# Performance work log

Measured on AMD Instinct MI355X. Metric: run time of the kernel, lower is better.

## Reference

```python
import jax, jax.numpy as jnp
import numpy as np
from jax.scipy.linalg import expm

LATENT, HIDDEN, N_PARTS, K = 128, 2048, 128, 2048
OMEGA_DIM, TRANZ_DIM = 9 * N_PARTS, 3 * N_PARTS


def setup_inputs() -> dict:
    key = jax.random.key(0)
    ks = jax.random.split(key, 10)

    def w(k, out_d, in_d):
        # eqx.nn.Linear-style scale ~ 1/sqrt(fan_in)
        return jax.random.normal(k, (out_d, in_d), dtype=jnp.float32) / np.sqrt(in_d)

    return {
        "x_init": jax.random.normal(ks[0], (LATENT, K), dtype=jnp.float32),
        "Wo0": w(ks[1], HIDDEN, LATENT),
        "Wo1": w(ks[2], HIDDEN, HIDDEN),
        "Wo2": w(ks[3], HIDDEN, HIDDEN),
        "Wo3": w(ks[4], OMEGA_DIM, HIDDEN),
        "Wt0": w(ks[5], HIDDEN, LATENT),
        "Wt1": w(ks[6], HIDDEN, HIDDEN),
        "Wt2": w(ks[7], HIDDEN, HIDDEN),
        "Wt3": w(ks[8], TRANZ_DIM, HIDDEN),
    }


def _mlp(weights, x):
    # bias-free MLP, relu on all but last layer; x is (d_in, K)
    for i, W in enumerate(weights):
        x = W @ x
        if i + 1 < len(weights):
            x = jax.nn.relu(x)
    return x


def reference(x_init, Wo0, Wo1, Wo2, Wo3, Wt0, Wt1, Wt2, Wt3):
    omega = _mlp([Wo0, Wo1, Wo2, Wo3], x_init)            # (9n, K)
    n = omega.shape[0] // 9
    k = omega.shape[1]
    # exp_omega 2D branch: vmap over columns, each column -> (n,3,3) expm batch
    mats = omega.T.reshape(k * n, 3, 3)
    R = jax.vmap(expm)(mats).reshape(k, 9 * n)            # (K, 9n)
    rotations = R.T                                        # (9n, K)
    translations = _mlp([Wt0, Wt1, Wt2, Wt3], x_init)     # (3n, K)
    # form_transformations (2D branch): stack translation as a 4th row -> (12n, K)
    rot_r = rotations.reshape(n, 3, 3, k)
    tr_r = translations.reshape(n, 1, 3, k)
    transf = jnp.concatenate([rot_r, tr_r], axis=1).reshape(-1, k)  # (12n, K)
    return (omega, transf, rotations, translations)
```

## Files before the change

kernel.cpp:

```cpp
#include <hip/hip_runtime.h>
#include <stdint.h>


typedef short bf16x8 __attribute__((ext_vector_type(8)));
typedef float f32x4 __attribute__((ext_vector_type(4)));

__device__ __forceinline__ unsigned short f2bf(float f) {
  unsigned int x = __float_as_uint(f);
  unsigned int r = (x + 0x7fffu + ((x >> 16) & 1u)) >> 16;
  return (unsigned short)r;
}

__device__ __forceinline__ void gld_lds16(const void* g, void* l) {
  __builtin_amdgcn_global_load_lds(
      (__attribute__((address_space(1))) void*)(g),
      (__attribute__((address_space(3))) void*)(l),
      16, 0, 0);
}

__global__ void prep_k(const float* __restrict__ x,
                       const float* __restrict__ wo0, const float* __restrict__ wo1,
                       const float* __restrict__ wo2, const float* __restrict__ wo3,
                       const float* __restrict__ wt0, const float* __restrict__ wt1,
                       const float* __restrict__ wt2, const float* __restrict__ wt3,
                       unsigned short* __restrict__ dst, unsigned short* __restrict__ xt) {
  __shared__ float tile[32][33];
  const int b = blockIdx.x;
  const int tid = threadIdx.x;
  if (b >= 9984) {
    const int r = b - 9984;
    const int bx = r & 63, by = r >> 6;
    const int tx = tid & 31, ty = tid >> 5;
#pragma unroll
    for (int i = 0; i < 32; i += 8)
      tile[ty + i][tx] = x[(size_t)(by * 32 + ty + i) * 2048 + bx * 32 + tx];
    __syncthreads();
#pragma unroll
    for (int i = 0; i < 32; i += 8)
      xt[(size_t)(bx * 32 + ty + i) * 128 + by * 32 + tx] = f2bf(tile[tx][ty + i]);
    return;
  }
  int idx = (b * 256 + tid) * 8;
  if (idx >= 20447232) return;
  const float* src;
  int off;
  if (idx < 8650752) {
    if (idx < 262144)       { src = wo0; off = idx; }
    else if (idx < 4456448) { src = wo1; off = idx - 262144; }
    else                    { src = wo2; off = idx - 4456448; }
  } else {
    if (idx < 11010048)      { src = wo3; off = idx - 8650752; }
    else if (idx < 11272192) { src = wt0; off = idx - 11010048; }
    else if (idx < 15466496) { src = wt1; off = idx - 11272192; }
    else if (idx < 19660800) { src = wt2; off = idx - 15466496; }
    else                     { src = wt3; off = idx - 19660800; }
  }
  float4 a = *(const float4*)(src + off);
  float4 c = *(const float4*)(src + off + 4);
  uint4 o;
  o.x = (unsigned)f2bf(a.x) | ((unsigned)f2bf(a.y) << 16);
  o.y = (unsigned)f2bf(a.z) | ((unsigned)f2bf(a.w) << 16);
  o.z = (unsigned)f2bf(c.x) | ((unsigned)f2bf(c.y) << 16);
  o.w = (unsigned)f2bf(c.z) | ((unsigned)f2bf(c.w) << 16);
  *(uint4*)(dst + idx) = o;
}

template <int SWZ>
__global__ __launch_bounds__(256, 2) void gemm_tn(
    const unsigned short* __restrict__ A0, const unsigned short* __restrict__ B0,
    unsigned short* __restrict__ C0, int n0tiles, int ldc0,
    const unsigned short* __restrict__ A1, const unsigned short* __restrict__ B1,
    unsigned short* __restrict__ C1, int ldc1, int K) {
  __shared__ alignas(16) unsigned short Asl[128 * 128];
  __shared__ alignas(16) unsigned short Bsl[128 * 128];

  int mt, yt;
  if (SWZ) {
    int id = blockIdx.x;
    int xcd = id & 7, s = id >> 3;
    mt = ((xcd & 1) << 3) + (s & 7);
    yt = ((xcd >> 1) << 3) + (s >> 3);
  } else {
    mt = blockIdx.x;
    yt = blockIdx.y;
  }

  const unsigned short* A;
  const unsigned short* B;
  unsigned short* C;
  int ldc;
  if (yt < n0tiles) { A = A0; B = B0; C = C0; ldc = ldc0; }
  else { A = A1; B = B1; C = C1; ldc = ldc1; yt -= n0tiles; }

  const unsigned short* Ab = A + (size_t)mt * 128 * K;
  const unsigned short* Bb = B + (size_t)yt * 128 * K;

  const int tid = threadIdx.x;
  const int wave = tid >> 6, lane = tid & 63;
  const int mw = (wave >> 1) * 64, nw = (wave & 1) * 64;
  const int l16 = lane & 15, quad = lane >> 4;

  f32x4 acc[4][4] = {};

  for (int k0 = 0; k0 < K; k0 += 128) {
#pragma unroll
    for (int i = 0; i < 8; ++i) {
      int c = i * 256 + tid;
      int row = c >> 4;
      int l = (c & 15) ^ (row & 15);
      gld_lds16(Ab + (size_t)row * K + k0 + l * 8, &Asl[c * 8]);
      gld_lds16(Bb + (size_t)row * K + k0 + l * 8, &Bsl[c * 8]);
    }
    __syncthreads();

#pragma unroll
    for (int h = 0; h < 4; ++h) {
      bf16x8 af[4], bfr[4];
#pragma unroll
      for (int t = 0; t < 4; ++t) {
        int row = mw + t * 16 + l16;
        int p = (h * 4 + quad) ^ (row & 15);
        af[t] = *(const bf16x8*)&Asl[row * 128 + p * 8];
      }
#pragma unroll
      for (int t = 0; t < 4; ++t) {
        int row = nw + t * 16 + l16;
        int p = (h * 4 + quad) ^ (row & 15);
        bfr[t] = *(const bf16x8*)&Bsl[row * 128 + p * 8];
      }
#pragma unroll
      for (int tm = 0; tm < 4; ++tm)
#pragma unroll
        for (int tn = 0; tn < 4; ++tn)
          acc[tm][tn] = __builtin_amdgcn_mfma_f32_16x16x32_bf16(af[tm], bfr[tn], acc[tm][tn], 0, 0, 0);
    }
    __syncthreads();
  }

  const int mbase = mt * 128 + mw;
  const int nbase = yt * 128 + nw;
#pragma unroll
  for (int tm = 0; tm < 4; ++tm) {
#pragma unroll
    for (int tn = 0; tn < 4; ++tn) {
      int col = nbase + tn * 16 + l16;
      int row0 = mbase + tm * 16 + quad * 4;
#pragma unroll
      for (int r = 0; r < 4; ++r) {
        float v = fmaxf(acc[tm][tn][r], 0.0f);
        C[(size_t)(row0 + r) * ldc + col] = f2bf(v);
      }
    }
  }
}

__device__ __forceinline__ void mm3(const float* a, const float* b, float* c) {
#pragma unroll
  for (int r = 0; r < 3; ++r)
#pragma unroll
    for (int cc = 0; cc < 3; ++cc)
      c[r * 3 + cc] = a[r * 3 + 0] * b[0 + cc] + a[r * 3 + 1] * b[3 + cc] + a[r * 3 + 2] * b[6 + cc];
}

__device__ __forceinline__ void expm3(const float* a, float* E) {
  float n1 = 0.f;
#pragma unroll
  for (int c = 0; c < 3; ++c) {
    float s = fabsf(a[c]) + fabsf(a[3 + c]) + fabsf(a[6 + c]);
    n1 = fmaxf(n1, s);
  }
  int s = 0;
  if (n1 > 0.25f) {
    s = (int)ceilf(log2f(n1 * 4.0f));
    if (s < 0) s = 0;
  }
  const float scl = exp2f((float)(-s));
  float As[9];
#pragma unroll
  for (int i = 0; i < 9; ++i) As[i] = a[i] * scl;
  float T[9] = {1, 0, 0, 0, 1, 0, 0, 0, 1};
#pragma unroll
  for (int i = 0; i < 9; ++i) E[i] = T[i];
#pragma unroll
  for (int t = 1; t <= 12; ++t) {
    float Tn[9];
    mm3(T, As, Tn);
    const float inv = 1.0f / (float)t;
#pragma unroll
    for (int i = 0; i < 9; ++i) { T[i] = Tn[i] * inv; E[i] += T[i]; }
  }
  for (int q = 0; q < s; ++q) {
    float Tn[9];
    mm3(E, E, Tn);
#pragma unroll
    for (int i = 0; i < 9; ++i) E[i] = Tn[i];
  }
}

__global__ __launch_bounds__(256, 2) void gemm_l3(
    const unsigned short* __restrict__ Ho, const unsigned short* __restrict__ W9,
    const unsigned short* __restrict__ Ht, const unsigned short* __restrict__ W3,
    float* __restrict__ out) {
  __shared__ alignas(16) char smem[16384 + 39168];
  unsigned short* Asl = (unsigned short*)smem;
  unsigned short* Bsl = (unsigned short*)(smem + 16384);
  float* Cl = (float*)(smem + 16384);

  const int mt = blockIdx.x;
  const int yt = blockIdx.y;
  const int tid = threadIdx.x;
  const int wave = tid >> 6, lane = tid & 63;
  const int l16 = lane & 15, quad = lane >> 4;
  const int mbase = mt * 64;

  float* omega  = out;
  float* transf = out + (size_t)1152 * 2048;
  float* rot    = out + (size_t)(1152 + 1536) * 2048;
  float* transl = out + (size_t)(1152 + 1536 + 1152) * 2048;

  if (yt < 8) {
    const unsigned short* Ab = Ho + (size_t)mbase * 2048;
    const unsigned short* Bb = W9 + (size_t)yt * 144 * 2048;
    const int mw = wave * 16;
    f32x4 acc[9] = {};

    for (int k0 = 0; k0 < 2048; k0 += 128) {
#pragma unroll
      for (int i = 0; i < 4; ++i) {
        int c = i * 256 + tid;
        int row = c >> 4;
        int l = (c & 15) ^ (row & 15);
        gld_lds16(Ab + (size_t)row * 2048 + k0 + l * 8, &Asl[c * 8]);
      }
#pragma unroll
      for (int i = 0; i < 9; ++i) {
        int c = i * 256 + tid;
        int row = c >> 4;
        int l = (c & 15) ^ (row & 15);
        gld_lds16(Bb + (size_t)row * 2048 + k0 + l * 8, &Bsl[c * 8]);
      }
      __syncthreads();
#pragma unroll
      for (int h = 0; h < 4; ++h) {
        bf16x8 af;
        {
          int row = mw + l16;
          int p = (h * 4 + quad) ^ (row & 15);
          af = *(const bf16x8*)&Asl[row * 128 + p * 8];
        }
#pragma unroll
        for (int t = 0; t < 9; ++t) {
          int row = t * 16 + l16;
          int p = (h * 4 + quad) ^ (row & 15);
          bf16x8 bf = *(const bf16x8*)&Bsl[row * 128 + p * 8];
          acc[t] = __builtin_amdgcn_mfma_f32_16x16x32_bf16(af, bf, acc[t], 0, 0, 0);
        }
      }
      __syncthreads();
    }

#pragma unroll
    for (int t = 0; t < 9; ++t) {
      int d = t * 16 + l16;
      int s0 = mw + quad * 4;
      *(f32x4*)&Cl[d * 68 + s0] = acc[t];
    }
    __syncthreads();

    const int jbase = yt * 16;
    const int k = mbase + lane;
#pragma unroll 1
    for (int pp = 0; pp < 4; ++pp) {
      int pl = wave * 4 + pp;
      int j = jbase + pl;
      float a[9];
#pragma unroll
      for (int i = 0; i < 9; ++i) a[i] = Cl[(pl * 9 + i) * 68 + lane];
#pragma unroll
      for (int i = 0; i < 9; ++i) omega[(size_t)(9 * j + i) * 2048 + k] = a[i];
      float E[9];
      expm3(a, E);
#pragma unroll
      for (int i = 0; i < 9; ++i) {
        rot[(size_t)(9 * j + i) * 2048 + k] = E[i];
        transf[(size_t)(12 * j + i) * 2048 + k] = E[i];
      }
    }
  } else {
    const int nt = yt - 8;
    const unsigned short* Ab = Ht + (size_t)mbase * 2048;
    const unsigned short* Bb = W3 + (size_t)nt * 128 * 2048;
    const int mw = (wave >> 1) * 32, nw = (wave & 1) * 64;
    f32x4 acc[2][4] = {};

    for (int k0 = 0; k0 < 2048; k0 += 128) {
#pragma unroll
      for (int i = 0; i < 4; ++i) {
        int c = i * 256 + tid;
        int row = c >> 4;
        int l = (c & 15) ^ (row & 15);
        gld_lds16(Ab + (size_t)row * 2048 + k0 + l * 8, &Asl[c * 8]);
      }
#pragma unroll
      for (int i = 0; i < 8; ++i) {
        int c = i * 256 + tid;
        int row = c >> 4;
        int l = (c & 15) ^ (row & 15);
        gld_lds16(Bb + (size_t)row * 2048 + k0 + l * 8, &Bsl[c * 8]);
      }
      __syncthreads();
#pragma unroll
      for (int h = 0; h < 4; ++h) {
        bf16x8 af[2], bfr[4];
#pragma unroll
        for (int t = 0; t < 2; ++t) {
          int row = mw + t * 16 + l16;
          int p = (h * 4 + quad) ^ (row & 15);
          af[t] = *(const bf16x8*)&Asl[row * 128 + p * 8];
        }
#pragma unroll
        for (int t = 0; t < 4; ++t) {
          int row = nw + t * 16 + l16;
          int p = (h * 4 + quad) ^ (row & 15);
          bfr[t] = *(const bf16x8*)&Bsl[row * 128 + p * 8];
        }
#pragma unroll
        for (int tm = 0; tm < 2; ++tm)
#pragma unroll
          for (int tn = 0; tn < 4; ++tn)
            acc[tm][tn] = __builtin_amdgcn_mfma_f32_16x16x32_bf16(af[tm], bfr[tn], acc[tm][tn], 0, 0, 0);
      }
      __syncthreads();
    }

    const int nbase = nt * 128 + nw;
#pragma unroll
    for (int tm = 0; tm < 2; ++tm) {
#pragma unroll
      for (int tn = 0; tn < 4; ++tn) {
        int n = nbase + tn * 16 + l16;
        int row0 = mbase + mw + tm * 16 + quad * 4;
        int j = n / 3, c = n % 3;
        *(f32x4*)&transl[(size_t)n * 2048 + row0] = acc[tm][tn];
        *(f32x4*)&transf[(size_t)(12 * j + 9 + c) * 2048 + row0] = acc[tm][tn];
      }
    }
  }
}

extern "C" void kernel_launch(void* const* d_in, const int* in_sizes, int n_in,
                              void* d_out, int out_size, void* d_ws, size_t ws_size,
                              hipStream_t stream) {
  const float* x   = (const float*)d_in[0];
  const float* Wo0 = (const float*)d_in[1];
  const float* Wo1 = (const float*)d_in[2];
  const float* Wo2 = (const float*)d_in[3];
  const float* Wo3 = (const float*)d_in[4];
  const float* Wt0 = (const float*)d_in[5];
  const float* Wt1 = (const float*)d_in[6];
  const float* Wt2 = (const float*)d_in[7];
  const float* Wt3 = (const float*)d_in[8];

  unsigned short* wb   = (unsigned short*)d_ws;
  unsigned short* wo0b = wb + 0;
  unsigned short* wo1b = wb + 262144;
  unsigned short* wo2b = wb + 4456448;
  unsigned short* wo3b = wb + 8650752;
  unsigned short* wt0b = wb + 11010048;
  unsigned short* wt1b = wb + 11272192;
  unsigned short* wt2b = wb + 15466496;
  unsigned short* wt3b = wb + 19660800;
  unsigned short* Xt   = wb + 20447232;
  unsigned short* HoA  = Xt + 262144;
  unsigned short* HoB  = HoA + 4194304;
  unsigned short* HtA  = HoB + 4194304;
  unsigned short* HtB  = HtA + 4194304;

  prep_k<<<10240, 256, 0, stream>>>(x, Wo0, Wo1, Wo2, Wo3, Wt0, Wt1, Wt2, Wt3, wb, Xt);

  gemm_tn<1><<<512, 256, 0, stream>>>(Xt, wo0b, HoA, 16, 2048,
                                      Xt, wt0b, HtA, 2048, 128);
  gemm_tn<1><<<512, 256, 0, stream>>>(HoA, wo1b, HoB, 16, 2048,
                                      HtA, wt1b, HtB, 2048, 2048);
  gemm_tn<1><<<512, 256, 0, stream>>>(HoB, wo2b, HoA, 16, 2048,
                                      HtB, wt2b, HtA, 2048, 2048);
  gemm_l3<<<dim3(32, 11), 256, 0, stream>>>(HoA, wo3b, HtA, wt3b, (float*)d_out);
}
```

Measured before the change: 239.2 us.

## Add 256x128-tile triple-buffered GEMM kernel for the two hidden layers

Adds a new bf16 MFMA GEMM kernel for the two 2048x2048 hidden layers. It uses 512 threads, a 256x128 output tile, a three-stage LDS ring filled by direct global-to-LDS loads with an XOR swizzle, and split half-K staging interleaved with MFMA and priority hints. The block index is mapped onto XCDs so tiles sharing operands land on the same XCD. The larger tile raises operand reuse and the deeper pipeline hides load latency. The cost is more LDS per block and fewer blocks (256), which may limit occupancy and load balance across CUs.

```diff
diff --git a/kernel.cpp b/kernel.cpp
--- a/kernel.cpp
+++ b/kernel.cpp
@@ -154,6 +154,130 @@
   }
 }
 
+__device__ __forceinline__ void stage_part8(const unsigned short* Ab,
+                                            const unsigned short* Bb,
+                                            unsigned short* As, unsigned short* Bs,
+                                            int k0, int tid, int part, int K) {
+#pragma unroll
+  for (int i = part * 2; i < part * 2 + 2; ++i) {
+    int c = i * 512 + tid;
+    int row = c >> 3, pc = c & 7;
+    int l = pc ^ (row & 7);
+    gld_lds16(Ab + (size_t)row * K + k0 + l * 8, As + c * 8);
+  }
+  {
+    int c = part * 512 + tid;
+    int row = c >> 3, pc = c & 7;
+    int l = pc ^ (row & 7);
+    gld_lds16(Bb + (size_t)row * K + k0 + l * 8, Bs + c * 8);
+  }
+}
+
+__device__ __forceinline__ bf16x8 ldfrag8(const unsigned short* S, int row, int p) {
+  return *(const bf16x8*)&S[row * 64 + ((p ^ (row & 7)) * 8)];
+}
+
+__global__ __launch_bounds__(512, 2) void gemm_tn8(
+    const unsigned short* __restrict__ A0, const unsigned short* __restrict__ B0,
+    unsigned short* __restrict__ C0,
+    const unsigned short* __restrict__ A1, const unsigned short* __restrict__ B1,
+    unsigned short* __restrict__ C1, int K) {
+  __shared__ alignas(16) unsigned short As[3][256 * 64];
+  __shared__ alignas(16) unsigned short Bs[3][128 * 64];
+
+  const int id = blockIdx.x;
+  const int xcd = id & 7, s = id >> 3;
+  const int mt = s & 7;
+  const int ntt = xcd * 4 + (s >> 3);
+
+  const unsigned short* A;
+  const unsigned short* B;
+  unsigned short* C;
+  int ntl;
+  if (ntt < 16) { A = A0; B = B0; C = C0; ntl = ntt; }
+  else          { A = A1; B = B1; C = C1; ntl = ntt - 16; }
+
+  const unsigned short* Ab = A + (size_t)mt * 256 * K;
+  const unsigned short* Bb = B + (size_t)ntl * 128 * K;
+
+  const int tid = threadIdx.x;
+  const int wave = tid >> 6, lane = tid & 63;
+  const int mw = (wave >> 1) * 64;
+  const int nw = (wave & 1) * 64;
+  const int l16 = lane & 15, quad = lane >> 4;
+
+  f32x4 acc[4][4] = {};
+  const int NT = K >> 6;
+
+  stage_part8(Ab, Bb, As[0], Bs[0], 0, tid, 0, K);
+  stage_part8(Ab, Bb, As[0], Bs[0], 0, tid, 1, K);
+  stage_part8(Ab, Bb, As[1], Bs[1], 64, tid, 0, K);
+  stage_part8(Ab, Bb, As[1], Bs[1], 64, tid, 1, K);
+  asm volatile("s_waitcnt vmcnt(6)" ::: "memory");
+  __builtin_amdgcn_s_barrier();
+
+  int cur = 0;
+  for (int t = 0; t < NT; ++t) {
+    asm volatile("" ::: "memory");
+    const int nxt2 = t + 2;
+    int s2 = cur + 2; if (s2 >= 3) s2 -= 3;
+    const int k2 = nxt2 << 6;
+
+    if (nxt2 < NT) stage_part8(Ab, Bb, As[s2], Bs[s2], k2, tid, 0, K);
+    bf16x8 a0[4], b0[4];
+#pragma unroll
+    for (int i = 0; i < 4; ++i) a0[i] = ldfrag8(&As[cur][0], mw + i * 16 + l16, quad);
+#pragma unroll
+    for (int i = 0; i < 4; ++i) b0[i] = ldfrag8(&Bs[cur][0], nw + i * 16 + l16, quad);
+    __builtin_amdgcn_s_barrier();
+    __builtin_amdgcn_s_setprio(1);
+#pragma unroll
+    for (int tm = 0; tm < 4; ++tm)
+#pragma unroll
+      for (int tn = 0; tn < 4; ++tn)
+        acc[tm][tn] = __builtin_amdgcn_mfma_f32_16x16x32_bf16(a0[tm], b0[tn], acc[tm][tn], 0, 0, 0);
+    __builtin_amdgcn_s_setprio(0);
+
+    if (nxt2 < NT) stage_part8(Ab, Bb, As[s2], Bs[s2], k2, tid, 1, K);
+    bf16x8 a1[4], b1[4];
+#pragma unroll
+    for (int i = 0; i < 4; ++i) a1[i] = ldfrag8(&As[cur][0], mw + i * 16 + l16, 4 + quad);
+#pragma unroll
+    for (int i = 0; i < 4; ++i) b1[i] = ldfrag8(&Bs[cur][0], nw + i * 16 + l16, 4 + quad);
+    __builtin_amdgcn_s_barrier();
+    __builtin_amdgcn_s_setprio(1);
+#pragma unroll
+    for (int tm = 0; tm < 4; ++tm)
+#pragma unroll
+      for (int tn = 0; tn < 4; ++tn)
+        acc[tm][tn] = __builtin_amdgcn_mfma_f32_16x16x32_bf16(a1[tm], b1[tn], acc[tm][tn], 0, 0, 0);
+    __builtin_amdgcn_s_setprio(0);
+
+    if (t + 1 < NT) {
+      if (nxt2 < NT) asm volatile("s_waitcnt vmcnt(6)" ::: "memory");
+      else           asm volatile("s_waitcnt vmcnt(0)" ::: "memory");
+      __builtin_amdgcn_s_barrier();
+    }
+    ++cur; if (cur >= 3) cur = 0;
+  }
+
+  const int mbase = mt * 256 + mw;
+  const int nbase = ntl * 128 + nw;
+#pragma unroll
+  for (int tm = 0; tm < 4; ++tm) {
+#pragma unroll
+    for (int tn = 0; tn < 4; ++tn) {
+      int col = nbase + tn * 16 + l16;
+      int row0 = mbase + tm * 16 + quad * 4;
+#pragma unroll
+      for (int r = 0; r < 4; ++r) {
+        float v = fmaxf(acc[tm][tn][r], 0.0f);
+        C[(size_t)(row0 + r) * 2048 + col] = f2bf(v);
+      }
+    }
+  }
+}
+
 __device__ __forceinline__ void mm3(const float* a, const float* b, float* c) {
 #pragma unroll
   for (int r = 0; r < 3; ++r)
@@ -380,9 +504,7 @@
 
   gemm_tn<1><<<512, 256, 0, stream>>>(Xt, wo0b, HoA, 16, 2048,
                                       Xt, wt0b, HtA, 2048, 128);
-  gemm_tn<1><<<512, 256, 0, stream>>>(HoA, wo1b, HoB, 16, 2048,
-                                      HtA, wt1b, HtB, 2048, 2048);
-  gemm_tn<1><<<512, 256, 0, stream>>>(HoB, wo2b, HoA, 16, 2048,
-                                      HtB, wt2b, HtA, 2048, 2048);
+  gemm_tn8<<<256, 512, 0, stream>>>(HoA, wo1b, HoB, HtA, wt1b, HtB, 2048);
+  gemm_tn8<<<256, 512, 0, stream>>>(HoB, wo2b, HoA, HtB, wt2b, HtA, 2048);
   gemm_l3<<<dim3(32, 11), 256, 0, stream>>>(HoA, wo3b, HtA, wt3b, (float*)d_out);
 }
```

Result: slower. 281.7 us (+17.8%).
